# Optimization experiments

Measured on AMD Instinct MI355X. Metric: run time of the kernel, lower is better.

The kernel has to match this reference:

```python
import jax, jax.numpy as jnp
import numpy as np

VOCAB = 4096   # vocab_size; must equal dim for weight + A@B to typecheck (as in source)
DIM = 4096
RANK = 256     # lora_rank
BATCH, SEQ = 4, 2048


def setup_inputs() -> dict:
    key = jax.random.key(0)
    k1, k2, k3, k4, k5 = jax.random.split(key, 5)
    x = jax.random.randint(k1, (BATCH, SEQ), 0, VOCAB)
    padding_mask = jax.random.randint(k2, (BATCH, SEQ), 0, 2).astype(bool)
    weight = jax.random.normal(k3, (VOCAB, DIM), dtype=jnp.float32) * 0.02
    A = jax.random.normal(k4, (VOCAB, RANK), dtype=jnp.float32) * 0.01
    B = jax.random.normal(k5, (RANK, VOCAB), dtype=jnp.float32) * 0.01
    return {"x": x, "padding_mask": padding_mask, "weight": weight, "A": A, "B": B}


def reference(x, padding_mask, weight, A, B):
    # world_size == 1, rank == 0 in the source module, so the distributed
    # index-shift / mask / all_reduce branches are no-ops.
    # lora_rank > 0 branch: embedding against the LoRA-corrected weight.
    # NOTE: faithful to source, A@B is [V, V] and requires DIM == VOCAB.
    corrected = weight + A @ B            # [V, DIM]
    y = corrected[x]                      # gather rows -> [B, S, DIM]
    # y[padding_mask] = 0
    y = jnp.where(padding_mask[..., None], jnp.zeros((), dtype=y.dtype), y)
    return y
```

## Files before the change

kernel.cpp:

```cpp
#include <hip/hip_runtime.h>
#include <stdint.h>

#define NTOK 8192
#define NCOL 4096
#define RANK 256
#define TPB  128
#define CPB  256

typedef __attribute__((ext_vector_type(8))) short bf16x8;
typedef __attribute__((ext_vector_type(4))) float f32x4;

__device__ __forceinline__ unsigned short f2bf(float f) {
    unsigned int u = __float_as_uint(f);
    u += 0x7fffu + ((u >> 16) & 1u);
    return (unsigned short)(u >> 16);
}

__device__ __forceinline__ void gload_lds16(const uint4* g, uint4* l) {
    __builtin_amdgcn_global_load_lds(
        (const __attribute__((address_space(1))) void*)g,
        (__attribute__((address_space(3))) void*)l, 16, 0, 0);
}

__global__ __launch_bounds__(256) void prep_kernel(
    const float* __restrict__ A, const float* __restrict__ B,
    unsigned short* __restrict__ Abf, unsigned short* __restrict__ Bfrag)
{
    if (blockIdx.x < 1024) {
        int i = blockIdx.x * 256 + threadIdx.x;
        float4 v = reinterpret_cast<const float4*>(A)[i];
        ushort4 o;
        o.x = f2bf(v.x); o.y = f2bf(v.y); o.z = f2bf(v.z); o.w = f2bf(v.w);
        reinterpret_cast<ushort4*>(Abf)[i] = o;
    } else {
        int gt = (blockIdx.x - 1024) * 256 + threadIdx.x;
        int ct = gt >> 9;
        int rem = gt & 511;
        int ks = rem >> 6;
        int ln = rem & 63;
        int col = ct * 16 + (ln & 15);
        int kb  = ks * 32 + ((ln >> 4) << 3);
        unsigned short pk[8];
        #pragma unroll
        for (int j = 0; j < 8; ++j)
            pk[j] = f2bf(B[(size_t)(kb + j) * NCOL + col]);
        uint4 o;
        o.x = (unsigned)pk[0] | ((unsigned)pk[1] << 16);
        o.y = (unsigned)pk[2] | ((unsigned)pk[3] << 16);
        o.z = (unsigned)pk[4] | ((unsigned)pk[5] << 16);
        o.w = (unsigned)pk[6] | ((unsigned)pk[7] << 16);
        reinterpret_cast<uint4*>(Bfrag)[gt] = o;
    }
}

__global__ __launch_bounds__(256) void emb_lora_mfma(
    const int* __restrict__ x,
    const int* __restrict__ mask,
    const float* __restrict__ W,
    const unsigned short* __restrict__ Abf,
    const unsigned short* __restrict__ Bfrag,
    float* __restrict__ out)
{
    __shared__ int s_idx[TPB];
    __shared__ int s_msk[TPB];
    __shared__ uint4 b_lds[2][512];

    const int tid  = threadIdx.x;
    const int lane = tid & 63;
    const int wave = tid >> 6;
    const int tok0 = blockIdx.x * TPB;
    const int col0 = blockIdx.y * CPB;

    if (tid < TPB) {
        s_idx[tid] = x[tok0 + tid];
        s_msk[tid] = mask[tok0 + tid];
    }
    __syncthreads();

    const int a0row = s_idx[wave * 32 + (lane & 15)];
    const int a1row = s_idx[wave * 32 + 16 + (lane & 15)];
    const unsigned short* ap0 = Abf + (size_t)a0row * RANK + ((lane >> 4) << 3);
    const unsigned short* ap1 = Abf + (size_t)a1row * RANK + ((lane >> 4) << 3);
    bf16x8 aA[8], aB[8];
    #pragma unroll
    for (int s = 0; s < 8; ++s) {
        aA[s] = *reinterpret_cast<const bf16x8*>(ap0 + s * 32);
        aB[s] = *reinterpret_cast<const bf16x8*>(ap1 + s * 32);
    }

    const int colb = col0 + (lane & 15);
    int msk0[4], msk1[4];
    unsigned woff0[4], woff1[4], ooff0[4], ooff1[4];
    #pragma unroll
    for (int r = 0; r < 4; ++r) {
        int row0 = wave * 32 + ((lane >> 4) << 2) + r;
        int row1 = row0 + 16;
        msk0[r] = s_msk[row0];
        msk1[r] = s_msk[row1];
        woff0[r] = (unsigned)s_idx[row0] * NCOL + colb;
        woff1[r] = (unsigned)s_idx[row1] * NCOL + colb;
        ooff0[r] = (unsigned)(tok0 + row0) * NCOL + colb;
        ooff1[r] = (unsigned)(tok0 + row1) * NCOL + colb;
    }

    const uint4* bpanel = reinterpret_cast<const uint4*>(Bfrag)
                          + (size_t)(blockIdx.y * 16) * 512;

    float wv0[4][4], wv1[4][4];
    #pragma unroll
    for (int p = 0; p < 4; ++p) {
        #pragma unroll
        for (int r = 0; r < 4; ++r) {
            float v0 = 0.0f, v1 = 0.0f;
            if (!msk0[r]) v0 = W[woff0[r] + p * 16];
            if (!msk1[r]) v1 = W[woff1[r] + p * 16];
            wv0[p][r] = v0;
            wv1[p][r] = v1;
        }
    }

#define STAGE(T, BUF)                                                    \
    {                                                                    \
        const uint4* gs = bpanel + (T) * 512 + wave * 128 + lane;        \
        gload_lds16(gs,      &b_lds[BUF][wave * 128]);                   \
        gload_lds16(gs + 64, &b_lds[BUF][wave * 128 + 64]);              \
    }

    STAGE(0, 0);
    __syncthreads();

#define TILE_BODY(T, BUF, SLOT, PF, LAST)                                \
    {                                                                    \
        const int t_ = (T);                                              \
         \
        float wc0[4], wc1[4];                                            \
        _Pragma("unroll")                                                \
        for (int r = 0; r < 4; ++r) { wc0[r] = wv0[SLOT][r]; wc1[r] = wv1[SLOT][r]; } \
        if (PF) {                                                        \
            _Pragma("unroll")                                            \
            for (int r = 0; r < 4; ++r) {                                \
                float v0 = 0.0f, v1 = 0.0f;                              \
                if (!msk0[r]) v0 = W[woff0[r] + (t_ + 4) * 16];          \
                if (!msk1[r]) v1 = W[woff1[r] + (t_ + 4) * 16];          \
                wv0[SLOT][r] = v0;                                       \
                wv1[SLOT][r] = v1;                                       \
            }                                                            \
        }                                                                \
        if (!(LAST)) { STAGE(t_ + 1, 1 - (BUF)); }                       \
                 \
        __builtin_amdgcn_sched_barrier(0);                               \
        uint4 bb[8];                                                     \
        _Pragma("unroll")                                                \
        for (int s = 0; s < 8; ++s)                                      \
            bb[s] = b_lds[BUF][s * 64 + lane];                           \
        f32x4 acc00 = {0.f,0.f,0.f,0.f}, acc01 = {0.f,0.f,0.f,0.f};      \
        f32x4 acc10 = {0.f,0.f,0.f,0.f}, acc11 = {0.f,0.f,0.f,0.f};      \
        _Pragma("unroll")                                                \
        for (int s = 0; s < 4; ++s) {                                    \
            bf16x8 b0 = __builtin_bit_cast(bf16x8, bb[s]);               \
            bf16x8 b1 = __builtin_bit_cast(bf16x8, bb[s + 4]);           \
            acc00 = __builtin_amdgcn_mfma_f32_16x16x32_bf16(aA[s],     b0, acc00, 0, 0, 0); \
            acc01 = __builtin_amdgcn_mfma_f32_16x16x32_bf16(aA[s + 4], b1, acc01, 0, 0, 0); \
            acc10 = __builtin_amdgcn_mfma_f32_16x16x32_bf16(aB[s],     b0, acc10, 0, 0, 0); \
            acc11 = __builtin_amdgcn_mfma_f32_16x16x32_bf16(aB[s + 4], b1, acc11, 0, 0, 0); \
        }                                                                \
        _Pragma("unroll")                                                \
        for (int r = 0; r < 4; ++r) {                                    \
            float v0 = msk0[r] ? 0.0f : (acc00[r] + acc01[r] + wc0[r]);  \
            float v1 = msk1[r] ? 0.0f : (acc10[r] + acc11[r] + wc1[r]);  \
            out[ooff0[r] + t_ * 16] = v0;                                \
            out[ooff1[r] + t_ * 16] = v1;                                \
        }                                                                \
        if (!(LAST)) {                                                   \
                               \
            asm volatile("s_waitcnt vmcnt(8)" ::: "memory");             \
            __builtin_amdgcn_s_barrier();                                \
        }                                                                \
    }

    TILE_BODY(0,  0, 0, 1, 0);
    TILE_BODY(1,  1, 1, 1, 0);
    TILE_BODY(2,  0, 2, 1, 0);
    TILE_BODY(3,  1, 3, 1, 0);
    TILE_BODY(4,  0, 0, 1, 0);
    TILE_BODY(5,  1, 1, 1, 0);
    TILE_BODY(6,  0, 2, 1, 0);
    TILE_BODY(7,  1, 3, 1, 0);
    TILE_BODY(8,  0, 0, 1, 0);
    TILE_BODY(9,  1, 1, 1, 0);
    TILE_BODY(10, 0, 2, 1, 0);
    TILE_BODY(11, 1, 3, 1, 0);
    TILE_BODY(12, 0, 0, 0, 0);
    TILE_BODY(13, 1, 1, 0, 0);
    TILE_BODY(14, 0, 2, 0, 0);
    TILE_BODY(15, 1, 3, 0, 1);
#undef TILE_BODY
#undef STAGE
}

extern "C" void kernel_launch(void* const* d_in, const int* in_sizes, int n_in,
                              void* d_out, int out_size, void* d_ws, size_t ws_size,
                              hipStream_t stream) {
    (void)in_sizes; (void)n_in; (void)out_size; (void)ws_size;

    const int*   x    = (const int*)d_in[0];
    const int*   mask = (const int*)d_in[1];
    const float* W    = (const float*)d_in[2];
    const float* A    = (const float*)d_in[3];
    const float* B    = (const float*)d_in[4];
    float*       out  = (float*)d_out;

    unsigned short* Abf   = (unsigned short*)d_ws;
    unsigned short* Bfrag = (unsigned short*)((char*)d_ws + (2u << 20));

    prep_kernel<<<dim3(1536), dim3(256), 0, stream>>>(A, B, Abf, Bfrag);

    dim3 grid(NTOK / TPB, NCOL / CPB);
    emb_lora_mfma<<<grid, dim3(256), 0, stream>>>(x, mask, W, Abf, Bfrag, out);
}
```

Measured before the change: 49.42 us.

## Precompute full LoRA product table once, then gather rows with a streaming kernel

Adds a path that first computes the whole A@B product (vocab x dim) once into a bf16 workspace table. A second, simple per-token kernel then gathers W and LoRA rows, adds them and zeroes masked tokens. This removes the redundant per-token GEMM, which repeats work for duplicated token ids, and halves the matrix-multiply FLOPs. In exchange it adds an extra kernel launch, a 32MB intermediate write and re-read, and bf16 rounding of the LoRA term. The old fused kernel is kept as a fallback for when the workspace is too small.

```diff
diff --git a/kernel.cpp b/kernel.cpp
--- a/kernel.cpp
+++ b/kernel.cpp
@@ -4,8 +4,6 @@
 #define NTOK 8192
 #define NCOL 4096
 #define RANK 256
-#define TPB  128
-#define CPB  256
 
 typedef __attribute__((ext_vector_type(8))) short bf16x8;
 typedef __attribute__((ext_vector_type(4))) float f32x4;
@@ -14,6 +12,9 @@
     unsigned int u = __float_as_uint(f);
     u += 0x7fffu + ((u >> 16) & 1u);
     return (unsigned short)(u >> 16);
+}
+__device__ __forceinline__ float bf2f(unsigned int u16) {
+    return __uint_as_float(u16 << 16);
 }
 
 __device__ __forceinline__ void gload_lds16(const uint4* g, uint4* l) {
@@ -53,28 +54,114 @@
     }
 }
 
-__global__ __launch_bounds__(256) void emb_lora_mfma(
+__global__ __launch_bounds__(256) void p1_gemm(
+    const unsigned short* __restrict__ Abf,
+    const unsigned short* __restrict__ Bfrag,
+    unsigned short* __restrict__ loraBf)
+{
+    const int tid  = threadIdx.x;
+    const int lane = tid & 63;
+    const int wave = tid >> 6;
+    const int row0 = blockIdx.x * 128;
+    const int col0 = blockIdx.y * 256;
+
+    const int a0row = row0 + wave * 32 + (lane & 15);
+    const int a1row = a0row + 16;
+    const unsigned short* ap0 = Abf + (size_t)a0row * RANK + ((lane >> 4) << 3);
+    const unsigned short* ap1 = Abf + (size_t)a1row * RANK + ((lane >> 4) << 3);
+    bf16x8 aA[8], aB[8];
+    #pragma unroll
+    for (int s = 0; s < 8; ++s) {
+        aA[s] = *reinterpret_cast<const bf16x8*>(ap0 + s * 32);
+        aB[s] = *reinterpret_cast<const bf16x8*>(ap1 + s * 32);
+    }
+
+    const int colb = col0 + (lane & 15);
+    const int rb0  = row0 + wave * 32 + ((lane >> 4) << 2);
+    unsigned obase0 = (unsigned)rb0 * NCOL + colb;
+    unsigned obase1 = (unsigned)(rb0 + 16) * NCOL + colb;
+
+    const uint4* bcol = reinterpret_cast<const uint4*>(Bfrag)
+                        + (size_t)(blockIdx.y * 16) * 512 + lane;
+
+    #pragma unroll 1
+    for (int t = 0; t < 16; ++t) {
+        uint4 bb[8];
+        #pragma unroll
+        for (int s = 0; s < 8; ++s)
+            bb[s] = bcol[t * 512 + s * 64];
+        f32x4 acc00 = {0.f,0.f,0.f,0.f}, acc01 = {0.f,0.f,0.f,0.f};
+        f32x4 acc10 = {0.f,0.f,0.f,0.f}, acc11 = {0.f,0.f,0.f,0.f};
+        #pragma unroll
+        for (int s = 0; s < 4; ++s) {
+            bf16x8 b0 = __builtin_bit_cast(bf16x8, bb[s]);
+            bf16x8 b1 = __builtin_bit_cast(bf16x8, bb[s + 4]);
+            acc00 = __builtin_amdgcn_mfma_f32_16x16x32_bf16(aA[s],     b0, acc00, 0, 0, 0);
+            acc01 = __builtin_amdgcn_mfma_f32_16x16x32_bf16(aA[s + 4], b1, acc01, 0, 0, 0);
+            acc10 = __builtin_amdgcn_mfma_f32_16x16x32_bf16(aB[s],     b0, acc10, 0, 0, 0);
+            acc11 = __builtin_amdgcn_mfma_f32_16x16x32_bf16(aB[s + 4], b1, acc11, 0, 0, 0);
+        }
+        #pragma unroll
+        for (int r = 0; r < 4; ++r) {
+            loraBf[obase0 + r * NCOL + t * 16] = f2bf(acc00[r] + acc01[r]);
+            loraBf[obase1 + r * NCOL + t * 16] = f2bf(acc10[r] + acc11[r]);
+        }
+    }
+}
+
+__global__ __launch_bounds__(256) void p2_gather(
     const int* __restrict__ x,
     const int* __restrict__ mask,
+    const float* __restrict__ W,
+    const unsigned short* __restrict__ loraBf,
+    float* __restrict__ out)
+{
+    const int tok = blockIdx.x;
+    const int tid = threadIdx.x;
+    float4* orow = reinterpret_cast<float4*>(out + (size_t)tok * NCOL) + tid;
+
+    if (mask[tok]) {
+        float4 z = {0.f, 0.f, 0.f, 0.f};
+        #pragma unroll
+        for (int k = 0; k < 4; ++k) orow[k * 256] = z;
+    } else {
+        const int idx = x[tok];
+        const float4* wrow = reinterpret_cast<const float4*>(
+            W + (size_t)idx * NCOL) + tid;
+        const uint2* lrow = reinterpret_cast<const uint2*>(
+            loraBf + (size_t)idx * NCOL) + tid;
+        #pragma unroll
+        for (int k = 0; k < 4; ++k) {
+            float4 wv = wrow[k * 256];
+            uint2  lv = lrow[k * 256];
+            float4 o;
+            o.x = wv.x + bf2f(lv.x & 0xffffu);
+            o.y = wv.y + bf2f(lv.x >> 16);
+            o.z = wv.z + bf2f(lv.y & 0xffffu);
+            o.w = wv.w + bf2f(lv.y >> 16);
+            orow[k * 256] = o;
+        }
+    }
+}
+
+__global__ __launch_bounds__(256) void emb_lora_fused_fb(
+    const int* __restrict__ x, const int* __restrict__ mask,
     const float* __restrict__ W,
     const unsigned short* __restrict__ Abf,
     const unsigned short* __restrict__ Bfrag,
     float* __restrict__ out)
 {
-    __shared__ int s_idx[TPB];
-    __shared__ int s_msk[TPB];
+    __shared__ int s_idx[128];
+    __shared__ int s_msk[128];
     __shared__ uint4 b_lds[2][512];
 
     const int tid  = threadIdx.x;
     const int lane = tid & 63;
     const int wave = tid >> 6;
-    const int tok0 = blockIdx.x * TPB;
-    const int col0 = blockIdx.y * CPB;
-
-    if (tid < TPB) {
-        s_idx[tid] = x[tok0 + tid];
-        s_msk[tid] = mask[tok0 + tid];
-    }
+    const int tok0 = blockIdx.x * 128;
+    const int col0 = blockIdx.y * 256;
+
+    if (tid < 128) { s_idx[tid] = x[tok0 + tid]; s_msk[tid] = mask[tok0 + tid]; }
     __syncthreads();
 
     const int a0row = s_idx[wave * 32 + (lane & 15)];
@@ -95,8 +182,7 @@
     for (int r = 0; r < 4; ++r) {
         int row0 = wave * 32 + ((lane >> 4) << 2) + r;
         int row1 = row0 + 16;
-        msk0[r] = s_msk[row0];
-        msk1[r] = s_msk[row1];
+        msk0[r] = s_msk[row0]; msk1[r] = s_msk[row1];
         woff0[r] = (unsigned)s_idx[row0] * NCOL + colb;
         woff1[r] = (unsigned)s_idx[row1] * NCOL + colb;
         ooff0[r] = (unsigned)(tok0 + row0) * NCOL + colb;
@@ -105,34 +191,29 @@
 
     const uint4* bpanel = reinterpret_cast<const uint4*>(Bfrag)
                           + (size_t)(blockIdx.y * 16) * 512;
-
     float wv0[4][4], wv1[4][4];
     #pragma unroll
-    for (int p = 0; p < 4; ++p) {
+    for (int p = 0; p < 4; ++p)
         #pragma unroll
         for (int r = 0; r < 4; ++r) {
             float v0 = 0.0f, v1 = 0.0f;
             if (!msk0[r]) v0 = W[woff0[r] + p * 16];
             if (!msk1[r]) v1 = W[woff1[r] + p * 16];
-            wv0[p][r] = v0;
-            wv1[p][r] = v1;
-        }
-    }
-
-#define STAGE(T, BUF)                                                    \
+            wv0[p][r] = v0; wv1[p][r] = v1;
+        }
+
+#define STAGE_FB(T, BUF)                                                 \
     {                                                                    \
         const uint4* gs = bpanel + (T) * 512 + wave * 128 + lane;        \
         gload_lds16(gs,      &b_lds[BUF][wave * 128]);                   \
         gload_lds16(gs + 64, &b_lds[BUF][wave * 128 + 64]);              \
     }
-
-    STAGE(0, 0);
+    STAGE_FB(0, 0);
     __syncthreads();
 
-#define TILE_BODY(T, BUF, SLOT, PF, LAST)                                \
+#define TILE_FB(T, BUF, SLOT, PF, LAST)                                  \
     {                                                                    \
         const int t_ = (T);                                              \
-         \
         float wc0[4], wc1[4];                                            \
         _Pragma("unroll")                                                \
         for (int r = 0; r < 4; ++r) { wc0[r] = wv0[SLOT][r]; wc1[r] = wv1[SLOT][r]; } \
@@ -142,17 +223,14 @@
                 float v0 = 0.0f, v1 = 0.0f;                              \
                 if (!msk0[r]) v0 = W[woff0[r] + (t_ + 4) * 16];          \
                 if (!msk1[r]) v1 = W[woff1[r] + (t_ + 4) * 16];          \
-                wv0[SLOT][r] = v0;                                       \
-                wv1[SLOT][r] = v1;                                       \
+                wv0[SLOT][r] = v0; wv1[SLOT][r] = v1;                    \
             }                                                            \
         }                                                                \
-        if (!(LAST)) { STAGE(t_ + 1, 1 - (BUF)); }                       \
-                 \
+        if (!(LAST)) { STAGE_FB(t_ + 1, 1 - (BUF)); }                    \
         __builtin_amdgcn_sched_barrier(0);                               \
         uint4 bb[8];                                                     \
         _Pragma("unroll")                                                \
-        for (int s = 0; s < 8; ++s)                                      \
-            bb[s] = b_lds[BUF][s * 64 + lane];                           \
+        for (int s = 0; s < 8; ++s) bb[s] = b_lds[BUF][s * 64 + lane];   \
         f32x4 acc00 = {0.f,0.f,0.f,0.f}, acc01 = {0.f,0.f,0.f,0.f};      \
         f32x4 acc10 = {0.f,0.f,0.f,0.f}, acc11 = {0.f,0.f,0.f,0.f};      \
         _Pragma("unroll")                                                \
@@ -172,36 +250,26 @@
             out[ooff1[r] + t_ * 16] = v1;                                \
         }                                                                \
         if (!(LAST)) {                                                   \
-                               \
             asm volatile("s_waitcnt vmcnt(8)" ::: "memory");             \
             __builtin_amdgcn_s_barrier();                                \
         }                                                                \
     }
-
-    TILE_BODY(0,  0, 0, 1, 0);
-    TILE_BODY(1,  1, 1, 1, 0);
-    TILE_BODY(2,  0, 2, 1, 0);
-    TILE_BODY(3,  1, 3, 1, 0);
-    TILE_BODY(4,  0, 0, 1, 0);
-    TILE_BODY(5,  1, 1, 1, 0);
-    TILE_BODY(6,  0, 2, 1, 0);
-    TILE_BODY(7,  1, 3, 1, 0);
-    TILE_BODY(8,  0, 0, 1, 0);
-    TILE_BODY(9,  1, 1, 1, 0);
-    TILE_BODY(10, 0, 2, 1, 0);
-    TILE_BODY(11, 1, 3, 1, 0);
-    TILE_BODY(12, 0, 0, 0, 0);
-    TILE_BODY(13, 1, 1, 0, 0);
-    TILE_BODY(14, 0, 2, 0, 0);
-    TILE_BODY(15, 1, 3, 0, 1);
-#undef TILE_BODY
-#undef STAGE
+    TILE_FB(0,  0, 0, 1, 0); TILE_FB(1,  1, 1, 1, 0);
+    TILE_FB(2,  0, 2, 1, 0); TILE_FB(3,  1, 3, 1, 0);
+    TILE_FB(4,  0, 0, 1, 0); TILE_FB(5,  1, 1, 1, 0);
+    TILE_FB(6,  0, 2, 1, 0); TILE_FB(7,  1, 3, 1, 0);
+    TILE_FB(8,  0, 0, 1, 0); TILE_FB(9,  1, 1, 1, 0);
+    TILE_FB(10, 0, 2, 1, 0); TILE_FB(11, 1, 3, 1, 0);
+    TILE_FB(12, 0, 0, 0, 0); TILE_FB(13, 1, 1, 0, 0);
+    TILE_FB(14, 0, 2, 0, 0); TILE_FB(15, 1, 3, 0, 1);
+#undef TILE_FB
+#undef STAGE_FB
 }
 
 extern "C" void kernel_launch(void* const* d_in, const int* in_sizes, int n_in,
                               void* d_out, int out_size, void* d_ws, size_t ws_size,
                               hipStream_t stream) {
-    (void)in_sizes; (void)n_in; (void)out_size; (void)ws_size;
+    (void)in_sizes; (void)n_in; (void)out_size;
 
     const int*   x    = (const int*)d_in[0];
     const int*   mask = (const int*)d_in[1];
@@ -215,6 +283,13 @@
 
     prep_kernel<<<dim3(1536), dim3(256), 0, stream>>>(A, B, Abf, Bfrag);
 
-    dim3 grid(NTOK / TPB, NCOL / CPB);
-    emb_lora_mfma<<<grid, dim3(256), 0, stream>>>(x, mask, W, Abf, Bfrag, out);
-}
+    const size_t need = (4u << 20) + (size_t)NCOL * NCOL * 2;
+    if (ws_size >= need) {
+        unsigned short* loraBf = (unsigned short*)((char*)d_ws + (4u << 20));
+        p1_gemm<<<dim3(32, 16), dim3(256), 0, stream>>>(Abf, Bfrag, loraBf);
+        p2_gather<<<dim3(NTOK), dim3(256), 0, stream>>>(x, mask, W, loraBf, out);
+    } else {
+        emb_lora_fused_fb<<<dim3(64, 16), dim3(256), 0, stream>>>(
+            x, mask, W, Abf, Bfrag, out);
+    }
+}
```

After: 62.83 us. 27.1% more time.
